# Optimization experiments

Measured on AMD Instinct MI355X. Metric: run time of the kernel, lower is better.

The kernel has to match this reference:

```python
import jax, jax.numpy as jnp
import numpy as np

NUM_HEADS = 16


def _rope(x_BHLd, freqs_cis):
    # x: [B,H,L,d], freqs_cis: [L, d//2, 2] (cos, sin)
    B, H, L, d = x_BHLd.shape
    xs = x_BHLd.reshape(B, H, L, d // 2, 2)
    fc = freqs_cis.reshape(1, 1, L, d // 2, 2)
    real = xs[..., 0] * fc[..., 0] - xs[..., 1] * fc[..., 1]
    imag = xs[..., 1] * fc[..., 0] + xs[..., 0] * fc[..., 1]
    return jnp.stack([real, imag], axis=-1).reshape(B, H, L, d)


def setup_inputs() -> dict:
    key = jax.random.key(0)
    k1, k2 = jax.random.split(key)
    B, L, D = 1, 4096, 1024
    d = D // NUM_HEADS
    x = jax.random.normal(k1, (B, L, D), dtype=jnp.float32)
    Wqkv = jax.random.normal(k2, (D, 3 * D), dtype=jnp.float32) * (D ** -0.5)
    bqkv = jnp.zeros((3 * D,), dtype=jnp.float32)
    # true rotary cos/sin table: [L, d//2, 2]
    base = 10000.0
    inv_freq = 1.0 / (base ** (jnp.arange(0, d, 2, dtype=jnp.float32) / d))  # [d//2]
    t = jnp.arange(L, dtype=jnp.float32)
    ang = jnp.outer(t, inv_freq)  # [L, d//2]
    freqs_cis = jnp.stack([jnp.cos(ang), jnp.sin(ang)], axis=-1)  # [L, d//2, 2]
    return {"x": x, "freqs_cis": freqs_cis, "Wqkv": Wqkv, "bqkv": bqkv}


def reference(x, freqs_cis, Wqkv, bqkv):
    B, L, D = x.shape
    H = NUM_HEADS
    d = D // H
    qkv = x @ Wqkv + bqkv  # [B,L,3D]
    q, k, v = jnp.split(qkv, 3, axis=-1)
    split = lambda t: t.reshape(B, L, H, d).transpose(0, 2, 1, 3)  # [B,H,L,d]
    q, k, v = split(q), split(k), split(v)
    q = _rope(q, freqs_cis)
    k = _rope(k, freqs_cis)
    scale = 1.0 / jnp.sqrt(jnp.asarray(d, dtype=q.dtype))
    scores = jnp.einsum('bhqd,bhkd->bhqk', q, k) * scale  # [B,H,L,L]
    causal = jnp.tril(jnp.ones((L, L), dtype=bool))
    scores = jnp.where(causal, scores, jnp.asarray(-jnp.inf, dtype=scores.dtype))
    probs = jax.nn.softmax(scores, axis=-1)
    out = jnp.einsum('bhqk,bhkd->bhqd', probs, v)  # [B,H,L,d]
    return out.transpose(0, 2, 1, 3).reshape(B, L, D)
```

## Files before the change

### kernel.cpp

```cpp
#include <hip/hip_runtime.h>

typedef short short8 __attribute__((ext_vector_type(8)));
typedef float f32x4 __attribute__((ext_vector_type(4)));
typedef unsigned short u16;
typedef unsigned short u16x4 __attribute__((ext_vector_type(4)));
typedef unsigned short u16x8 __attribute__((ext_vector_type(8)));

#define L_SEQ 4096
#define NHEAD 16
#define HDIM  64
#define DMODEL 1024
#define N3    3072
#define HL    (L_SEQ * HDIM)

__device__ __forceinline__ u16 f2bf(float f) {
  union { float f; unsigned u; } v; v.f = f;
  return (u16)((v.u + 0x7fffu + ((v.u >> 16) & 1u)) >> 16);
}

__device__ __forceinline__ unsigned cvt_pk_bf16(float lo, float hi) {
  unsigned r;
  asm("v_cvt_pk_bf16_f32 %0, %1, %2" : "=v"(r) : "v"(lo), "v"(hi));
  return r;
}

__device__ __forceinline__ void gl2lds16(const void* g, void* l) {
  __builtin_amdgcn_global_load_lds(
      (const __attribute__((address_space(1))) unsigned int*)g,
      (__attribute__((address_space(3))) unsigned int*)l, 16, 0, 0);
}

__device__ __forceinline__ float fexp2(float x) { return __builtin_amdgcn_exp2f(x); }

__global__ void cvt_x_kernel(const float* __restrict__ x, u16* __restrict__ xb) {
  int i = blockIdx.x * blockDim.x + threadIdx.x;
  const f32x4* p = (const f32x4*)x + (size_t)i * 2;
  f32x4 a = p[0], b = p[1];
  u16x8 o;
  o[0] = f2bf(a[0]); o[1] = f2bf(a[1]); o[2] = f2bf(a[2]); o[3] = f2bf(a[3]);
  o[4] = f2bf(b[0]); o[5] = f2bf(b[1]); o[6] = f2bf(b[2]); o[7] = f2bf(b[3]);
  ((u16x8*)xb)[i] = o;
}

__global__ void cvt_wt_kernel(const float* __restrict__ W, u16* __restrict__ Wt) {
  __shared__ float t[64][65];
  int k0 = blockIdx.x * 64, n0 = blockIdx.y * 64;
  int tr = threadIdx.x >> 4;
  int tc = (threadIdx.x & 15) * 4;
  for (int rr = tr; rr < 64; rr += 16) {
    f32x4 v = *(const f32x4*)&W[(size_t)(k0 + rr) * N3 + n0 + tc];
    t[rr][tc] = v[0]; t[rr][tc + 1] = v[1]; t[rr][tc + 2] = v[2]; t[rr][tc + 3] = v[3];
  }
  __syncthreads();
  for (int rr = tr; rr < 64; rr += 16) {
    u16x4 o;
    o[0] = f2bf(t[tc + 0][rr]); o[1] = f2bf(t[tc + 1][rr]);
    o[2] = f2bf(t[tc + 2][rr]); o[3] = f2bf(t[tc + 3][rr]);
    *(u16x4*)&Wt[(size_t)(n0 + rr) * DMODEL + k0 + tc] = o;
  }
}

#define GBM 128
#define GBN 128
#define GBK 64

__global__ __launch_bounds__(256, 2) void gemm_qkv_kernel(
    const u16* __restrict__ xb, const u16* __restrict__ wt,
    const float* __restrict__ bias, const float* __restrict__ freqs,
    u16* __restrict__ Qb, u16* __restrict__ Kb, u16* __restrict__ Vt) {
  __shared__ u16 Asm[GBM * GBK];
  __shared__ u16 Bsm[GBN * GBK];
  const int tid = threadIdx.x, lane = tid & 63, wid = tid >> 6;
  const int lr = lane & 15, lh = lane >> 4;
  const int bx = blockIdx.x % (N3 / GBN), by = blockIdx.x / (N3 / GBN);
  const int m0 = by * GBM, n0 = bx * GBN;
  const int wr = wid >> 1, wc = wid & 1;
  const char* xbB = (const char*)xb;
  const char* wtB = (const char*)wt;
  char* AsmB = (char*)Asm;
  char* BsmB = (char*)Bsm;

  int pbase[4]; size_t srcAoff[4], srcBoff[4];
#pragma unroll
  for (int i = 0; i < 4; i++) {
    int p = wid * 4096 + i * 1024 + lane * 16;
    int row = p >> 7, slot = (p & 127) >> 4;
    int sw = (slot ^ (row & 7)) * 16;
    pbase[i] = p;
    srcAoff[i] = (size_t)(m0 + row) * (DMODEL * 2) + sw;
    srcBoff[i] = (size_t)(n0 + row) * (DMODEL * 2) + sw;
  }

  int aoff[4][2], boff[4][2];
#pragma unroll
  for (int mi = 0; mi < 4; mi++) {
    int row = wr * 64 + mi * 16 + lr;
#pragma unroll
    for (int kc = 0; kc < 2; kc++)
      aoff[mi][kc] = row * 128 + ((kc * 64 + lh * 16) ^ ((row & 7) << 4));
  }
#pragma unroll
  for (int ni = 0; ni < 4; ni++) {
    int row = wc * 64 + ni * 16 + lr;
#pragma unroll
    for (int kc = 0; kc < 2; kc++)
      boff[ni][kc] = row * 128 + ((kc * 64 + lh * 16) ^ ((row & 7) << 4));
  }

  f32x4 acc[4][4] = {};

  for (int k0 = 0; k0 < DMODEL; k0 += GBK) {
    __syncthreads();
#pragma unroll
    for (int i = 0; i < 4; i++) {
      gl2lds16(xbB + srcAoff[i] + (size_t)k0 * 2, AsmB + pbase[i]);
      gl2lds16(wtB + srcBoff[i] + (size_t)k0 * 2, BsmB + pbase[i]);
    }
    __syncthreads();
#pragma unroll
    for (int kc = 0; kc < 2; kc++) {
      short8 a[4], b[4];
#pragma unroll
      for (int mi = 0; mi < 4; mi++) a[mi] = *(const short8*)(AsmB + aoff[mi][kc]);
#pragma unroll
      for (int ni = 0; ni < 4; ni++) b[ni] = *(const short8*)(BsmB + boff[ni][kc]);
#pragma unroll
      for (int mi = 0; mi < 4; mi++)
#pragma unroll
        for (int ni = 0; ni < 4; ni++)
          acc[mi][ni] = __builtin_amdgcn_mfma_f32_16x16x32_bf16(a[mi], b[ni], acc[mi][ni], 0, 0, 0);
    }
  }

  const float QSCALE = 0.125f * 1.44269504088896f;
  const int colbase = n0 + wc * 64;
#pragma unroll
  for (int ni = 0; ni < 4; ni++) {
    int col = colbase + ni * 16 + lr;
    float bv = bias[col];
    int sect = col >> 10;
    int cc = col & 1023;
    int h = cc >> 6, j = cc & 63;
#pragma unroll
    for (int mi = 0; mi < 4; mi++) {
      int row0 = m0 + wr * 64 + mi * 16 + lh * 4;
      float v[4];
#pragma unroll
      for (int r = 0; r < 4; r++) v[r] = acc[mi][ni][r] + bv;
      if (sect < 2) {
        int i2 = j >> 1;
        bool odd = (j & 1) != 0;
#pragma unroll
        for (int r = 0; r < 4; r++) {
          float pv = __shfl_xor(v[r], 1);
          float2 cs = *(const float2*)&freqs[((size_t)(row0 + r) * 32 + i2) * 2];
          v[r] = odd ? (v[r] * cs.x + pv * cs.y) : (v[r] * cs.x - pv * cs.y);
          if (sect == 0) v[r] *= QSCALE;
        }
        u16* dst = (sect == 0 ? Qb : Kb) + (size_t)h * HL + (size_t)row0 * HDIM + j;
#pragma unroll
        for (int r = 0; r < 4; r++) dst[(size_t)r * HDIM] = f2bf(v[r]);
      } else {
        u16x4 o;
#pragma unroll
        for (int r = 0; r < 4; r++) o[r] = f2bf(v[r]);
        *(u16x4*)&Vt[(size_t)h * HL + (size_t)j * L_SEQ + row0] = o;
      }
    }
  }
}

#define QBLK 64
#define KBLK 64

__global__ __launch_bounds__(256, 4) void flash_kernel(
    const u16* __restrict__ Qb, const u16* __restrict__ Kb,
    const u16* __restrict__ Vt, float* __restrict__ out) {
  __shared__ char Ksm[2][KBLK * 128];
  __shared__ char Vsm[2][HDIM * KBLK * 2];
  __shared__ char Psm[4][16 * 128];
  const int tid = threadIdx.x, lane = tid & 63, wid = tid >> 6;
  const int lr = lane & 15, lh = lane >> 4;
  const int bid = blockIdx.x;
  const int h = bid & 15;
  const int s = bid >> 4;
  const int qb = (s & 1) ? (63 - (s >> 1)) : (s >> 1);
  const int q0 = qb * QBLK;
  const char* Qh = (const char*)(Qb + (size_t)h * HL);
  const char* Kh = (const char*)(Kb + (size_t)h * HL);
  const char* Vh = (const char*)(Vt + (size_t)h * HL);

  short8 qa[2];
  {
    int row = q0 + wid * 16 + lr;
#pragma unroll
    for (int kc = 0; kc < 2; kc++)
      qa[kc] = *(const short8*)(Qh + (size_t)row * 128 + kc * 64 + lh * 16);
  }

  f32x4 o[4] = {};
  float m_r = -__builtin_inff(), ls = 0.f;

  const int wmin = q0 + wid * 16;
  const int qrow = wmin + lr;
  char* Pw = Psm[wid];

  int pOff[2], KsrcOff[2], VsrcOff[2];
#pragma unroll
  for (int i = 0; i < 2; i++) {
    int p = wid * 2048 + i * 1024 + lane * 16;
    int row = p >> 7, slot = (p & 127) >> 4;
    int sw = (slot ^ (row & 7)) << 4;
    pOff[i] = p;
    KsrcOff[i] = row * 128 + sw;
    VsrcOff[i] = row * (L_SEQ * 2) + sw;
  }

  const int nt = qb + 1;

#pragma unroll
  for (int i = 0; i < 2; i++) {
    gl2lds16(Kh + KsrcOff[i], Ksm[0] + pOff[i]);
    gl2lds16(Vh + VsrcOff[i], Vsm[0] + pOff[i]);
  }
  __syncthreads();

  for (int t = 0; t < nt; ++t) {
    const int kt = t * KBLK;
    const int cur = t & 1;
    if (t + 1 < nt) {
      const size_t kn128 = (size_t)(kt + KBLK) * 128;
      const size_t kn2 = (size_t)(kt + KBLK) * 2;
#pragma unroll
      for (int i = 0; i < 2; i++) {
        gl2lds16(Kh + kn128 + KsrcOff[i], Ksm[cur ^ 1] + pOff[i]);
        gl2lds16(Vh + kn2 + VsrcOff[i], Vsm[cur ^ 1] + pOff[i]);
      }
    }
    const char* Kc = Ksm[cur];
    const char* Vc = Vsm[cur];

    f32x4 sfr[4];
    __builtin_amdgcn_s_setprio(1);
#pragma unroll
    for (int ni = 0; ni < 4; ni++) {
      int row = ni * 16 + lr;
      short8 bk0 = *(const short8*)(Kc + row * 128 + ((lh * 16) ^ ((row & 7) << 4)));
      short8 bk1 = *(const short8*)(Kc + row * 128 + ((64 + lh * 16) ^ ((row & 7) << 4)));
      f32x4 z = {};
      z = __builtin_amdgcn_mfma_f32_16x16x32_bf16(bk0, qa[0], z, 0, 0, 0);
      z = __builtin_amdgcn_mfma_f32_16x16x32_bf16(bk1, qa[1], z, 0, 0, 0);
      sfr[ni] = z;
    }
    __builtin_amdgcn_s_setprio(0);

    if (kt + KBLK - 1 > wmin) {
#pragma unroll
      for (int ni = 0; ni < 4; ni++)
#pragma unroll
        for (int r = 0; r < 4; r++)
          if (kt + ni * 16 + lh * 4 + r > qrow) sfr[ni][r] = -__builtin_inff();
    }

    float pmax = sfr[0][0];
#pragma unroll
    for (int ni = 0; ni < 4; ni++)
#pragma unroll
      for (int r = 0; r < 4; r++) pmax = fmaxf(pmax, sfr[ni][r]);
    pmax = fmaxf(pmax, __shfl_xor(pmax, 16));
    pmax = fmaxf(pmax, __shfl_xor(pmax, 32));

    if (__any(pmax > m_r + 8.f)) {
      float mn = fmaxf(m_r, pmax);
      float alpha = fexp2(m_r - mn);
      m_r = mn;
      ls *= alpha;
      float ao[4];
#pragma unroll
      for (int r = 0; r < 4; r++) ao[r] = __shfl(alpha, (lane & 48) | (lh * 4 + r));
#pragma unroll
      for (int vn = 0; vn < 4; vn++)
#pragma unroll
        for (int r = 0; r < 4; r++) o[vn][r] *= ao[r];
    }

    float psum = 0.f;
    unsigned Wp[4][2];
#pragma unroll
    for (int ni = 0; ni < 4; ni++) {
      float p0 = fexp2(sfr[ni][0] - m_r);
      float p1 = fexp2(sfr[ni][1] - m_r);
      float p2 = fexp2(sfr[ni][2] - m_r);
      float p3 = fexp2(sfr[ni][3] - m_r);
      psum += (p0 + p1) + (p2 + p3);
      Wp[ni][0] = cvt_pk_bf16(p0, p1);
      Wp[ni][1] = cvt_pk_bf16(p2, p3);
    }
    ls += psum;

#pragma unroll
    for (int ni = 0; ni < 4; ni++) {
      uint2 w2; w2.x = Wp[ni][0]; w2.y = Wp[ni][1];
      *(uint2*)(Pw + lr * 128 + ((ni * 32 + lh * 8) ^ ((lr & 7) << 4))) = w2;
    }
    asm volatile("s_waitcnt lgkmcnt(0)" ::: "memory");

    __builtin_amdgcn_s_setprio(1);
#pragma unroll
    for (int pc = 0; pc < 2; pc++) {
      short8 pa = *(const short8*)(Pw + lr * 128 + ((pc * 64 + lh * 16) ^ ((lr & 7) << 4)));
#pragma unroll
      for (int vn = 0; vn < 4; vn++) {
        int vrow = vn * 16 + lr;
        short8 bv = *(const short8*)(Vc + vrow * 128 + ((pc * 64 + lh * 16) ^ ((vrow & 7) << 4)));
        o[vn] = __builtin_amdgcn_mfma_f32_16x16x32_bf16(pa, bv, o[vn], 0, 0, 0);
      }
    }
    __builtin_amdgcn_s_setprio(0);

    __syncthreads();
  }

  ls += __shfl_xor(ls, 16);
  ls += __shfl_xor(ls, 32);
  float inv = 1.0f / ls;
  float invo[4];
#pragma unroll
  for (int r = 0; r < 4; r++) invo[r] = __shfl(inv, (lane & 48) | (lh * 4 + r));
#pragma unroll
  for (int r = 0; r < 4; r++) {
    int rowv = wmin + lh * 4 + r;
    float* op = out + (size_t)rowv * DMODEL + h * HDIM;
#pragma unroll
    for (int vn = 0; vn < 4; vn++) op[vn * 16 + lr] = o[vn][r] * invo[r];
  }
}

extern "C" void kernel_launch(void* const* d_in, const int* in_sizes, int n_in,
                              void* d_out, int out_size, void* d_ws, size_t ws_size,
                              hipStream_t stream) {
  const float* x = (const float*)d_in[0];
  const float* freqs = (const float*)d_in[1];
  const float* W = (const float*)d_in[2];
  const float* bias = (const float*)d_in[3];
  float* out = (float*)d_out;

  char* ws = (char*)d_ws;
  u16* xb = (u16*)ws;
  u16* wt = (u16*)(ws + 8u * 1024 * 1024);
  u16* Qb = (u16*)(ws + 14u * 1024 * 1024);
  u16* Kb = (u16*)(ws + 22u * 1024 * 1024);
  u16* Vt = (u16*)(ws + 30u * 1024 * 1024);

  cvt_x_kernel<<<2048, 256, 0, stream>>>(x, xb);
  cvt_wt_kernel<<<dim3(16, 48), 256, 0, stream>>>(W, wt);
  gemm_qkv_kernel<<<768, 256, 0, stream>>>(xb, wt, bias, freqs, Qb, Kb, Vt);
  flash_kernel<<<1024, 256, 0, stream>>>(Qb, Kb, Vt, out);
}
```

Before: 140.7 us.

## Double flash-attention query tile so each wave processes two 16-row groups

Increases the query block to 128 rows so each wave handles two 16-row query groups that share each K/V tile loaded into LDS. The K and V fragments read from LDS are reused across both groups, which halves K/V global and LDS traffic per query row and doubles MFMA work per sync. In exchange the grid is halved to 512 blocks, register use roughly doubles, and occupancy is lowered to 2 blocks per SM in launch bounds. Causal load balancing is kept by pairing short and long query tiles.

```diff
diff --git a/kernel.cpp b/kernel.cpp
--- a/kernel.cpp
+++ b/kernel.cpp
@@ -170,39 +170,45 @@
   }
 }
 
-#define QBLK 64
+#define QBLK 128
 #define KBLK 64
 
-__global__ __launch_bounds__(256, 4) void flash_kernel(
+__global__ __launch_bounds__(256, 2) void flash_kernel(
     const u16* __restrict__ Qb, const u16* __restrict__ Kb,
     const u16* __restrict__ Vt, float* __restrict__ out) {
   __shared__ char Ksm[2][KBLK * 128];
   __shared__ char Vsm[2][HDIM * KBLK * 2];
-  __shared__ char Psm[4][16 * 128];
+  __shared__ char Psm[4][32 * 128];
   const int tid = threadIdx.x, lane = tid & 63, wid = tid >> 6;
   const int lr = lane & 15, lh = lane >> 4;
   const int bid = blockIdx.x;
   const int h = bid & 15;
   const int s = bid >> 4;
-  const int qb = (s & 1) ? (63 - (s >> 1)) : (s >> 1);
-  const int q0 = qb * QBLK;
+  const int qt = (s < 16) ? s : (47 - s);
+  const int q0 = qt * QBLK;
   const char* Qh = (const char*)(Qb + (size_t)h * HL);
   const char* Kh = (const char*)(Kb + (size_t)h * HL);
   const char* Vh = (const char*)(Vt + (size_t)h * HL);
 
-  short8 qa[2];
-  {
-    int row = q0 + wid * 16 + lr;
+  const int wbase = q0 + wid * 32;
+
+  short8 qa[2][2];
+#pragma unroll
+  for (int hf = 0; hf < 2; hf++) {
+    int row = wbase + hf * 16 + lr;
 #pragma unroll
     for (int kc = 0; kc < 2; kc++)
-      qa[kc] = *(const short8*)(Qh + (size_t)row * 128 + kc * 64 + lh * 16);
-  }
-
-  f32x4 o[4] = {};
-  float m_r = -__builtin_inff(), ls = 0.f;
-
-  const int wmin = q0 + wid * 16;
-  const int qrow = wmin + lr;
+      qa[hf][kc] = *(const short8*)(Qh + (size_t)row * 128 + kc * 64 + lh * 16);
+  }
+
+  f32x4 o[2][4] = {};
+  float m_r[2], ls[2];
+  int qrow[2];
+#pragma unroll
+  for (int hf = 0; hf < 2; hf++) {
+    m_r[hf] = -__builtin_inff(); ls[hf] = 0.f;
+    qrow[hf] = wbase + hf * 16 + lr;
+  }
   char* Pw = Psm[wid];
 
   int pOff[2], KsrcOff[2], VsrcOff[2];
@@ -216,7 +222,7 @@
     VsrcOff[i] = row * (L_SEQ * 2) + sw;
   }
 
-  const int nt = qb + 1;
+  const int nt = 2 * qt + 2;
 
 #pragma unroll
   for (int i = 0; i < 2; i++) {
@@ -240,80 +246,102 @@
     const char* Kc = Ksm[cur];
     const char* Vc = Vsm[cur];
 
-    f32x4 sfr[4];
-    __builtin_amdgcn_s_setprio(1);
+    short8 bk[4][2];
 #pragma unroll
     for (int ni = 0; ni < 4; ni++) {
       int row = ni * 16 + lr;
-      short8 bk0 = *(const short8*)(Kc + row * 128 + ((lh * 16) ^ ((row & 7) << 4)));
-      short8 bk1 = *(const short8*)(Kc + row * 128 + ((64 + lh * 16) ^ ((row & 7) << 4)));
-      f32x4 z = {};
-      z = __builtin_amdgcn_mfma_f32_16x16x32_bf16(bk0, qa[0], z, 0, 0, 0);
-      z = __builtin_amdgcn_mfma_f32_16x16x32_bf16(bk1, qa[1], z, 0, 0, 0);
-      sfr[ni] = z;
-    }
+      bk[ni][0] = *(const short8*)(Kc + row * 128 + ((lh * 16) ^ ((row & 7) << 4)));
+      bk[ni][1] = *(const short8*)(Kc + row * 128 + ((64 + lh * 16) ^ ((row & 7) << 4)));
+    }
+
+    f32x4 sfr[2][4];
+    __builtin_amdgcn_s_setprio(1);
+#pragma unroll
+    for (int hf = 0; hf < 2; hf++)
+#pragma unroll
+      for (int ni = 0; ni < 4; ni++) {
+        f32x4 z = {};
+        z = __builtin_amdgcn_mfma_f32_16x16x32_bf16(bk[ni][0], qa[hf][0], z, 0, 0, 0);
+        z = __builtin_amdgcn_mfma_f32_16x16x32_bf16(bk[ni][1], qa[hf][1], z, 0, 0, 0);
+        sfr[hf][ni] = z;
+      }
     __builtin_amdgcn_s_setprio(0);
 
-    if (kt + KBLK - 1 > wmin) {
+#pragma unroll
+    for (int hf = 0; hf < 2; hf++) {
+      if (kt + KBLK - 1 > wbase + hf * 16) {
+#pragma unroll
+        for (int ni = 0; ni < 4; ni++)
+#pragma unroll
+          for (int r = 0; r < 4; r++)
+            if (kt + ni * 16 + lh * 4 + r > qrow[hf]) sfr[hf][ni][r] = -__builtin_inff();
+      }
+    }
+
+    float pmax[2];
+#pragma unroll
+    for (int hf = 0; hf < 2; hf++) {
+      float mx = sfr[hf][0][0];
 #pragma unroll
       for (int ni = 0; ni < 4; ni++)
 #pragma unroll
-        for (int r = 0; r < 4; r++)
-          if (kt + ni * 16 + lh * 4 + r > qrow) sfr[ni][r] = -__builtin_inff();
-    }
-
-    float pmax = sfr[0][0];
-#pragma unroll
-    for (int ni = 0; ni < 4; ni++)
-#pragma unroll
-      for (int r = 0; r < 4; r++) pmax = fmaxf(pmax, sfr[ni][r]);
-    pmax = fmaxf(pmax, __shfl_xor(pmax, 16));
-    pmax = fmaxf(pmax, __shfl_xor(pmax, 32));
-
-    if (__any(pmax > m_r + 8.f)) {
-      float mn = fmaxf(m_r, pmax);
-      float alpha = fexp2(m_r - mn);
-      m_r = mn;
-      ls *= alpha;
-      float ao[4];
-#pragma unroll
-      for (int r = 0; r < 4; r++) ao[r] = __shfl(alpha, (lane & 48) | (lh * 4 + r));
-#pragma unroll
-      for (int vn = 0; vn < 4; vn++)
-#pragma unroll
-        for (int r = 0; r < 4; r++) o[vn][r] *= ao[r];
-    }
-
-    float psum = 0.f;
-    unsigned Wp[4][2];
-#pragma unroll
-    for (int ni = 0; ni < 4; ni++) {
-      float p0 = fexp2(sfr[ni][0] - m_r);
-      float p1 = fexp2(sfr[ni][1] - m_r);
-      float p2 = fexp2(sfr[ni][2] - m_r);
-      float p3 = fexp2(sfr[ni][3] - m_r);
-      psum += (p0 + p1) + (p2 + p3);
-      Wp[ni][0] = cvt_pk_bf16(p0, p1);
-      Wp[ni][1] = cvt_pk_bf16(p2, p3);
-    }
-    ls += psum;
-
-#pragma unroll
-    for (int ni = 0; ni < 4; ni++) {
-      uint2 w2; w2.x = Wp[ni][0]; w2.y = Wp[ni][1];
-      *(uint2*)(Pw + lr * 128 + ((ni * 32 + lh * 8) ^ ((lr & 7) << 4))) = w2;
+        for (int r = 0; r < 4; r++) mx = fmaxf(mx, sfr[hf][ni][r]);
+      mx = fmaxf(mx, __shfl_xor(mx, 16));
+      mx = fmaxf(mx, __shfl_xor(mx, 32));
+      pmax[hf] = mx;
+    }
+
+    bool need = (pmax[0] > m_r[0] + 8.f) || (pmax[1] > m_r[1] + 8.f);
+    if (__any(need)) {
+#pragma unroll
+      for (int hf = 0; hf < 2; hf++) {
+        float mn = fmaxf(m_r[hf], pmax[hf]);
+        float alpha = fexp2(m_r[hf] - mn);
+        m_r[hf] = mn;
+        ls[hf] *= alpha;
+        float ao[4];
+#pragma unroll
+        for (int r = 0; r < 4; r++) ao[r] = __shfl(alpha, (lane & 48) | (lh * 4 + r));
+#pragma unroll
+        for (int vn = 0; vn < 4; vn++)
+#pragma unroll
+          for (int r = 0; r < 4; r++) o[hf][vn][r] *= ao[r];
+      }
+    }
+
+#pragma unroll
+    for (int hf = 0; hf < 2; hf++) {
+      float psum = 0.f;
+#pragma unroll
+      for (int ni = 0; ni < 4; ni++) {
+        float p0 = fexp2(sfr[hf][ni][0] - m_r[hf]);
+        float p1 = fexp2(sfr[hf][ni][1] - m_r[hf]);
+        float p2 = fexp2(sfr[hf][ni][2] - m_r[hf]);
+        float p3 = fexp2(sfr[hf][ni][3] - m_r[hf]);
+        psum += (p0 + p1) + (p2 + p3);
+        uint2 w2;
+        w2.x = cvt_pk_bf16(p0, p1);
+        w2.y = cvt_pk_bf16(p2, p3);
+        *(uint2*)(Pw + (hf * 16 + lr) * 128 + ((ni * 32 + lh * 8) ^ ((lr & 7) << 4))) = w2;
+      }
+      ls[hf] += psum;
     }
     asm volatile("s_waitcnt lgkmcnt(0)" ::: "memory");
 
     __builtin_amdgcn_s_setprio(1);
 #pragma unroll
     for (int pc = 0; pc < 2; pc++) {
-      short8 pa = *(const short8*)(Pw + lr * 128 + ((pc * 64 + lh * 16) ^ ((lr & 7) << 4)));
+      short8 pa[2];
+#pragma unroll
+      for (int hf = 0; hf < 2; hf++)
+        pa[hf] = *(const short8*)(Pw + (hf * 16 + lr) * 128 + ((pc * 64 + lh * 16) ^ ((lr & 7) << 4)));
 #pragma unroll
       for (int vn = 0; vn < 4; vn++) {
         int vrow = vn * 16 + lr;
         short8 bv = *(const short8*)(Vc + vrow * 128 + ((pc * 64 + lh * 16) ^ ((vrow & 7) << 4)));
-        o[vn] = __builtin_amdgcn_mfma_f32_16x16x32_bf16(pa, bv, o[vn], 0, 0, 0);
+#pragma unroll
+        for (int hf = 0; hf < 2; hf++)
+          o[hf][vn] = __builtin_amdgcn_mfma_f32_16x16x32_bf16(pa[hf], bv, o[hf][vn], 0, 0, 0);
       }
     }
     __builtin_amdgcn_s_setprio(0);
@@ -321,18 +349,22 @@
     __syncthreads();
   }
 
-  ls += __shfl_xor(ls, 16);
-  ls += __shfl_xor(ls, 32);
-  float inv = 1.0f / ls;
-  float invo[4];
-#pragma unroll
-  for (int r = 0; r < 4; r++) invo[r] = __shfl(inv, (lane & 48) | (lh * 4 + r));
-#pragma unroll
-  for (int r = 0; r < 4; r++) {
-    int rowv = wmin + lh * 4 + r;
-    float* op = out + (size_t)rowv * DMODEL + h * HDIM;
-#pragma unroll
-    for (int vn = 0; vn < 4; vn++) op[vn * 16 + lr] = o[vn][r] * invo[r];
+#pragma unroll
+  for (int hf = 0; hf < 2; hf++) {
+    float t = ls[hf];
+    t += __shfl_xor(t, 16);
+    t += __shfl_xor(t, 32);
+    float inv = 1.0f / t;
+    float invo[4];
+#pragma unroll
+    for (int r = 0; r < 4; r++) invo[r] = __shfl(inv, (lane & 48) | (lh * 4 + r));
+#pragma unroll
+    for (int r = 0; r < 4; r++) {
+      int rowv = wbase + hf * 16 + lh * 4 + r;
+      float* op = out + (size_t)rowv * DMODEL + h * HDIM;
+#pragma unroll
+      for (int vn = 0; vn < 4; vn++) op[vn * 16 + lr] = o[hf][vn][r] * invo[r];
+    }
   }
 }
 
@@ -355,5 +387,5 @@
   cvt_x_kernel<<<2048, 256, 0, stream>>>(x, xb);
   cvt_wt_kernel<<<dim3(16, 48), 256, 0, stream>>>(W, wt);
   gemm_qkv_kernel<<<768, 256, 0, stream>>>(xb, wt, bias, freqs, Qb, Kb, Vt);
-  flash_kernel<<<1024, 256, 0, stream>>>(Qb, Kb, Vt, out);
-}
+  flash_kernel<<<512, 256, 0, stream>>>(Qb, Kb, Vt, out);
+}
```

After: 150.8 us. 1.07x slower.
